# Kernel tuning notes

Measured on AMD Instinct MI355X. Metric: run time of the kernel, lower is better.

Reference implementation:

```python
import jax, jax.numpy as jnp
import numpy as np

EPS = 1e-5
NEG_SLOPE = 0.2  # DGL GATConv default leaky_relu slope


def conv1d_same(x, w, b):
    # x: [N, Cin, T], w: [Cout, Cin, K]
    y = jax.lax.conv_general_dilated(x, w, (1,), 'SAME',
                                     dimension_numbers=('NCW', 'OIW', 'NCW'))
    return y + b[None, :, None]


def gated_conv(x, w1, b1, w2, b2, w3, b3):
    # Temporal_Gated_Conv: relu(conv1(x)*sigmoid(conv2(x)) + conv3(x))
    return jax.nn.relu(conv1d_same(x, w1, b1) * jax.nn.sigmoid(conv1d_same(x, w2, b2))
                       + conv1d_same(x, w3, b3))


def bn3(x, g, b):
    # BatchNorm1d on [N, C, T]: stats over (N, T), training mode (batch stats)
    m = jnp.mean(x, (0, 2), keepdims=True)
    v = jnp.var(x, (0, 2), keepdims=True)
    return (x - m) * jax.lax.rsqrt(v + EPS) * g[None, :, None] + b[None, :, None]


def bn2(x, g, b):
    # BatchNorm1d on [N, F]: stats over N
    m = jnp.mean(x, 0, keepdims=True)
    v = jnp.var(x, 0, keepdims=True)
    return (x - m) * jax.lax.rsqrt(v + EPS) * g[None, :] + b[None, :]


def setup_inputs() -> dict:
    key = jax.random.key(0)
    ks = jax.random.split(key, 24)
    N, C, T, H, DEG = 20000, 32, 8, 4, 16
    F = C * T          # GAT in/out feats per head = 256
    E = N * DEG
    s = 0.05
    inp = {
        'X': jax.random.normal(ks[0], (N, C, T), jnp.float32),
        'src': jax.random.randint(ks[1], (E,), 0, N, jnp.int32),
        'dst': jax.random.randint(ks[2], (E,), 0, N, jnp.int32),
        # residual_proj: Conv1d(C->C, k=1)
        'rp_w': jax.random.normal(ks[3], (C, C, 1), jnp.float32) * s,
        'rp_b': jnp.zeros((C,), jnp.float32),
        # gated_conv1: three Conv1d(C->C, k=3)
        'g1_w1': jax.random.normal(ks[4], (C, C, 3), jnp.float32) * s,
        'g1_b1': jnp.zeros((C,), jnp.float32),
        'g1_w2': jax.random.normal(ks[5], (C, C, 3), jnp.float32) * s,
        'g1_b2': jnp.zeros((C,), jnp.float32),
        'g1_w3': jax.random.normal(ks[6], (C, C, 3), jnp.float32) * s,
        'g1_b3': jnp.zeros((C,), jnp.float32),
        'bn0_g': jnp.ones((C,), jnp.float32),
        'bn0_b': jnp.zeros((C,), jnp.float32),
        # GATConv: fc [H*F, F], attn_l/attn_r [H, F], bias [H*F]
        'gat_w': jax.random.normal(ks[7], (H * F, F), jnp.float32) * s,
        'attn_l': jax.random.normal(ks[8], (H, F), jnp.float32) * s,
        'attn_r': jax.random.normal(ks[9], (H, F), jnp.float32) * s,
        'gat_bias': jnp.zeros((H * F,), jnp.float32),
        'bn1_g': jnp.ones((H * F,), jnp.float32),
        'bn1_b': jnp.zeros((H * F,), jnp.float32),
        # gated_conv2: three Conv1d(C*H -> C, k=3)
        'g2_w1': jax.random.normal(ks[10], (C, C * H, 3), jnp.float32) * s,
        'g2_b1': jnp.zeros((C,), jnp.float32),
        'g2_w2': jax.random.normal(ks[11], (C, C * H, 3), jnp.float32) * s,
        'g2_b2': jnp.zeros((C,), jnp.float32),
        'g2_w3': jax.random.normal(ks[12], (C, C * H, 3), jnp.float32) * s,
        'g2_b3': jnp.zeros((C,), jnp.float32),
        'bn2_g': jnp.ones((C,), jnp.float32),
        'bn2_b': jnp.zeros((C,), jnp.float32),
    }
    return inp


def reference(X, src, dst, rp_w, rp_b, g1_w1, g1_b1, g1_w2, g1_b2, g1_w3, g1_b3,
              bn0_g, bn0_b, gat_w, attn_l, attn_r, gat_bias, bn1_g, bn1_b,
              g2_w1, g2_b1, g2_w2, g2_b2, g2_w3, g2_b3, bn2_g, bn2_b):
    N, C, T = X.shape
    H, F = attn_l.shape

    residual = conv1d_same(X, rp_w, rp_b)                      # [N, C, T]
    x = gated_conv(X, g1_w1, g1_b1, g1_w2, g1_b2, g1_w3, g1_b3)
    x = bn3(x, bn0_g, bn0_b)
    x = x.reshape(N, C * T)                                    # row-major flatten == torch .view

    # --- DGL GATConv (feat_drop=attn_drop=0, concat heads, ReLU activation) ---
    h = (x @ gat_w.T).reshape(N, H, F)                         # fc projection
    el = jnp.sum(h * attn_l, -1)                               # [N, H]
    er = jnp.sum(h * attn_r, -1)                               # [N, H]
    e = jax.nn.leaky_relu(el[src] + er[dst], NEG_SLOPE)        # [E, H]
    # segment softmax over incoming edges of each dst node
    m = jax.ops.segment_max(e, dst, num_segments=N)            # [N, H]
    ee = jnp.exp(e - m[dst])
    den = jax.ops.segment_sum(ee, dst, num_segments=N)         # [N, H]
    alpha = ee / den[dst]                                      # [E, H]
    rst = jax.ops.segment_sum(alpha[:, :, None] * h[src], dst, num_segments=N)  # [N, H, F]
    rst = jax.nn.relu(rst + gat_bias.reshape(H, F))

    x = rst.reshape(N, H * F)                                  # concat heads
    x = bn2(x, bn1_g, bn1_b)
    x = x.reshape(N, (H * F) // T, T)                          # [N, C*H, T]
    x = gated_conv(x, g2_w1, g2_b1, g2_w2, g2_b2, g2_w3, g2_b3)
    x = bn3(x, bn2_g, bn2_b)
    x = jax.nn.relu(x + residual)                              # self.last=True, dropout=0
    return x
```

## Files before the change

### kernel.cpp

```cpp
#include <hip/hip_runtime.h>
#include <stdint.h>

#define NN 20000
#define NE 320000

typedef unsigned short us16;
typedef __attribute__((ext_vector_type(8))) short short8;
typedef __attribute__((ext_vector_type(4))) float f32x4;

union U4 { uint4 v; us16 s[8]; unsigned u[4]; };
union U2 { uint2 v; us16 s[4]; };

__device__ __forceinline__ float b2f(us16 u){ return __uint_as_float(((unsigned)u)<<16); }
__device__ __forceinline__ us16 f2b(float f){
  unsigned u = __float_as_uint(f);
  u += 0x7fffu + ((u>>16)&1u);
  return (us16)(u>>16);
}

__global__ __launch_bounds__(256) void k_misc(
    const float* __restrict__ gatw, us16* __restrict__ Wb,
    const float* __restrict__ w1, const float* __restrict__ w2, const float* __restrict__ w3,
    us16* __restrict__ Wt,
    const float* __restrict__ c1w1, const float* __restrict__ c1w2, const float* __restrict__ c1w3,
    const float* __restrict__ rp_w, us16* __restrict__ Wt1,
    const float* __restrict__ attnl, const float* __restrict__ attnr,
    float* __restrict__ wl, float* __restrict__ wr,
    const int* __restrict__ dst, int* __restrict__ counts)
{
  const int b = blockIdx.x, tid = threadIdx.x;
  if(b < 256){
    int i = b*256 + tid;
    float4 v = *(const float4*)(gatw + (size_t)i*4);
    U2 o;
    o.s[0]=f2b(v.x); o.s[1]=f2b(v.y); o.s[2]=f2b(v.z); o.s[3]=f2b(v.w);
    *(uint2*)(Wb + (size_t)i*4) = o.v;
  } else if(b < 400){
    int i = (b-256)*256 + tid;
    int s = i/12288, rem = i%12288;
    int co3 = rem>>7, ci = rem&127;
    const float* w = (co3<32) ? w1 : (co3<64) ? w2 : w3;
    Wt[i] = f2b(w[(co3&31)*384 + ci*3 + s]);
  } else if(b < 448){
    int i = (b-400)*256 + tid;
    int s = i>>12, rem = i&4095;
    int co3 = rem>>5, ci = rem&31;
    float v;
    if(co3 < 96){
      const float* w = (co3<32) ? c1w1 : (co3<64) ? c1w2 : c1w3;
      v = w[(co3&31)*96 + ci*3 + s];
    } else {
      v = (s==1) ? rp_w[(co3-96)*32 + ci] : 0.f;
    }
    Wt1[i] = f2b(v);
  } else if(b < 480){
    int bb = b-448;
    int sel = bb>>4, hd = (bb>>2)&3, fq = bb&3;
    const float* attn = sel ? attnr : attnl;
    int k = tid;
    float s = 0.f;
    int f0 = fq*64;
    #pragma unroll 8
    for(int f=f0; f<f0+64; f++)
      s = fmaf(attn[hd*256+f], gatw[(size_t)(hd*256+f)*256 + k], s);
    atomicAdd(&((sel ? wr : wl)[hd*256+k]), s);
  } else {
    int e = (b-480)*256 + tid;
    if(e < NE) atomicAdd(&counts[dst[e]], 1);
  }
}

__global__ __launch_bounds__(256) void k_gemm1(
    const float* __restrict__ X, const us16* __restrict__ Wt1,
    const float* __restrict__ b1, const float* __restrict__ b2, const float* __restrict__ b3,
    const float* __restrict__ rp_b,
    us16* __restrict__ gc1, us16* __restrict__ resid,
    float* __restrict__ bn0_sum, float* __restrict__ bn0_sq,
    const int* __restrict__ counts, int* __restrict__ offsets, int* __restrict__ cursor)
{
  __shared__ float smemF[5760];
  __shared__ float redS[32], redQ[32];
  __shared__ int wred[4];
  const int tid = threadIdx.x;
  if(blockIdx.x < 1250){
    us16* As = (us16*)smemF;
    us16* Bs = As + 6400;
    if(tid<32){ redS[tid]=0.f; redQ[tid]=0.f; }
    const int node0 = blockIdx.x*16;
    const int lane = tid&63, wv = tid>>6;
    const int mrow = lane&15, kg = (lane>>4)*8;
    for(int idx=tid; idx<1024; idx+=256){
      int n = idx>>6, rem = idx&63, slot = (rem>>5)*9, ci = rem&31;
      As[n*400 + slot*40 + ci] = 0;
    }
    #pragma unroll
    for(int i=0;i<4;i++){
      int idx = i*256 + tid;
      int n = idx>>6, rem = idx&63, ci = rem>>1, tq = rem&1;
      float4 xv = *(const float4*)(X + (size_t)(node0+n)*256 + ci*8 + tq*4);
      us16* p = &As[n*400 + (tq*4+1)*40 + ci];
      p[0]   = f2b(xv.x);
      p[40]  = f2b(xv.y);
      p[80]  = f2b(xv.z);
      p[120] = f2b(xv.w);
    }
    f32x4 acc[2][8] = {};
    for(int s=0; s<3; s++){
      if(s) __syncthreads();
      #pragma unroll
      for(int i=0;i<2;i++){
        int c = i*256 + tid;
        int co = c>>2, cq = c&3;
        *(uint4*)&Bs[co*40 + cq*8] = *(const uint4*)(Wt1 + s*4096 + co*32 + cq*8);
      }
      __syncthreads();
      short8 af[2], bfr[8];
      #pragma unroll
      for(int i=0;i<2;i++){
        int r = wv*32 + i*16 + mrow;
        af[i] = *(const short8*)&As[(r>>3)*400 + ((r&7)+s)*40 + kg];
      }
      #pragma unroll
      for(int j=0;j<8;j++)
        bfr[j] = *(const short8*)&Bs[(j*16 + mrow)*40 + kg];
      #pragma unroll
      for(int i=0;i<2;i++){
        #pragma unroll
        for(int j=0;j<8;j++)
          acc[i][j] = __builtin_amdgcn_mfma_f32_16x16x32_bf16(af[i], bfr[j], acc[i][j], 0, 0, 0);
      }
    }
    __syncthreads();
    us16* Og = (us16*)smemF;
    us16* Or = Og + 4096;
    const int coA = lane&15, coB = coA+16;
    const float b1A=b1[coA], b2A=b2[coA], b3A=b3[coA], brA=rp_b[coA];
    const float b1B=b1[coB], b2B=b2[coB], b3B=b3[coB], brB=rp_b[coB];
    float sA=0.f, qA=0.f, sB=0.f, qB=0.f;
    const int g = lane>>4;
    #pragma unroll
    for(int i=0;i<2;i++){
      int node = wv*4 + i*2 + (g>>1);
      int t0 = (g&1)*4;
      U2 pA, pB, rA2, rB2;
      #pragma unroll
      for(int r=0;r<4;r++){
        float c1 = acc[i][0][r]+b1A, c2 = acc[i][2][r]+b2A, c3 = acc[i][4][r]+b3A;
        float rr = acc[i][6][r]+brA;
        float sg = 1.f/(1.f+__expf(-c2));
        float v = fmaf(c1,sg,c3); v = v>0.f ? v : 0.f;
        sA += v; qA += v*v;
        pA.s[r]=f2b(v); rA2.s[r]=f2b(rr);
        c1 = acc[i][1][r]+b1B; c2 = acc[i][3][r]+b2B; c3 = acc[i][5][r]+b3B;
        rr = acc[i][7][r]+brB;
        sg = 1.f/(1.f+__expf(-c2));
        v = fmaf(c1,sg,c3); v = v>0.f ? v : 0.f;
        sB += v; qB += v*v;
        pB.s[r]=f2b(v); rB2.s[r]=f2b(rr);
      }
      *(uint2*)&Og[node*256 + coA*8 + t0] = pA.v;
      *(uint2*)&Og[node*256 + coB*8 + t0] = pB.v;
      *(uint2*)&Or[node*256 + coA*8 + t0] = rA2.v;
      *(uint2*)&Or[node*256 + coB*8 + t0] = rB2.v;
    }
    sA += __shfl_xor(sA,16,64); sA += __shfl_xor(sA,32,64);
    qA += __shfl_xor(qA,16,64); qA += __shfl_xor(qA,32,64);
    sB += __shfl_xor(sB,16,64); sB += __shfl_xor(sB,32,64);
    qB += __shfl_xor(qB,16,64); qB += __shfl_xor(qB,32,64);
    if(lane < 16){
      atomicAdd(&redS[coA], sA); atomicAdd(&redQ[coA], qA);
      atomicAdd(&redS[coB], sB); atomicAdd(&redQ[coB], qB);
    }
    __syncthreads();
    #pragma unroll
    for(int i=0;i<2;i++){
      int idx = i*256 + tid;
      *(uint4*)(gc1   + (size_t)node0*256 + (size_t)idx*8) = *(const uint4*)&Og[idx*8];
      *(uint4*)(resid + (size_t)node0*256 + (size_t)idx*8) = *(const uint4*)&Or[idx*8];
    }
    if(tid<32)      atomicAdd(&bn0_sum[tid], redS[tid]);
    else if(tid<64) atomicAdd(&bn0_sq[tid-32], redQ[tid-32]);
  } else {
    const int lane = tid&63, wv = tid>>6;
    int running = 0;
    int4 cur;
    {
      int idx = tid*4;
      cur = *(const int4*)(counts + idx);
    }
    for(int t=0; t<20; t++){
      int4 nxt; nxt.x=0; nxt.y=0; nxt.z=0; nxt.w=0;
      if(t < 19){
        int idx = (t+1)*1024 + tid*4;
        if(idx+3 < NN) nxt = *(const int4*)(counts + idx);
        else {
          if(idx   < NN) nxt.x = counts[idx];
          if(idx+1 < NN) nxt.y = counts[idx+1];
          if(idx+2 < NN) nxt.z = counts[idx+2];
          if(idx+3 < NN) nxt.w = counts[idx+3];
        }
      }
      int s = cur.x + cur.y + cur.z + cur.w;
      int incl = s;
      #pragma unroll
      for(int off=1; off<64; off<<=1){
        int v = __shfl_up(incl, off, 64);
        if(lane >= off) incl += v;
      }
      if(lane==63) wred[wv] = incl;
      __syncthreads();
      int woff = 0, btot = 0;
      #pragma unroll
      for(int w2=0; w2<4; w2++){
        int x = wred[w2];
        btot += x;
        if(w2 < wv) woff += x;
      }
      int e0 = running + woff + incl - s;
      int idx = t*1024 + tid*4;
      int4 o; o.x=e0; o.y=e0+cur.x; o.z=o.y+cur.y; o.w=o.z+cur.z;
      if(idx+3 < NN){
        *(int4*)(offsets+idx) = o;
        *(int4*)(cursor+idx)  = o;
      } else {
        if(idx   < NN){ offsets[idx]  =o.x; cursor[idx]  =o.x; }
        if(idx+1 < NN){ offsets[idx+1]=o.y; cursor[idx+1]=o.y; }
        if(idx+2 < NN){ offsets[idx+2]=o.z; cursor[idx+2]=o.z; }
        if(idx+3 < NN){ offsets[idx+3]=o.w; cursor[idx+3]=o.w; }
      }
      running += btot;
      cur = nxt;
      __syncthreads();
    }
    if(tid==0) offsets[NN] = running;
  }
}

__global__ __launch_bounds__(256) void k_eler2(const us16* __restrict__ gc1,
    const float* __restrict__ bn0_sum, const float* __restrict__ bn0_sq,
    const float* __restrict__ bn0g, const float* __restrict__ bn0b,
    const float* __restrict__ wl, const float* __restrict__ wr,
    float* __restrict__ el, float* __restrict__ er)
{
  __shared__ float sa[32], sb[32];
  const int tid = threadIdx.x;
  if(tid<32){
    float m = bn0_sum[tid]*(1.f/160000.f);
    float v = bn0_sq[tid]*(1.f/160000.f) - m*m;
    float a = bn0g[tid]*rsqrtf(v + 1e-5f);
    sa[tid] = a; sb[tid] = bn0b[tid] - m*a;
  }
  __syncthreads();
  const int wv = tid>>6, lane = tid&63;
  const int node = blockIdx.x*4 + wv;
  U2 g; g.v = *(const uint2*)(gc1 + (size_t)node*256 + lane*4);
  const float a = sa[lane>>1], b = sb[lane>>1];
  float xv[4];
  #pragma unroll
  for(int j=0;j<4;j++) xv[j] = fmaf(a, b2f(g.s[j]), b);
  float res[8];
  #pragma unroll
  for(int hd=0; hd<4; hd++){
    float4 lv = *(const float4*)(wl + hd*256 + lane*4);
    float4 rv = *(const float4*)(wr + hd*256 + lane*4);
    res[hd]   = xv[0]*lv.x + xv[1]*lv.y + xv[2]*lv.z + xv[3]*lv.w;
    res[4+hd] = xv[0]*rv.x + xv[1]*rv.y + xv[2]*rv.z + xv[3]*rv.w;
  }
  #pragma unroll
  for(int o=32;o;o>>=1){
    #pragma unroll
    for(int k=0;k<8;k++) res[k] += __shfl_xor(res[k], o, 64);
  }
  if(lane==0){
    #pragma unroll
    for(int hd=0;hd<4;hd++){ el[node*4+hd]=res[hd]; er[node*4+hd]=res[4+hd]; }
  }
}

__global__ __launch_bounds__(256) void k_scatter(const int* __restrict__ src, const int* __restrict__ dst,
    int* __restrict__ cursor, int* __restrict__ esrc,
    const float* __restrict__ el, const float* __restrict__ er,
    float* __restrict__ ew)
{
  int e = blockIdx.x*256 + threadIdx.x;
  if(e < NE){
    int s = src[e], d = dst[e];
    int pos = atomicAdd(&cursor[d], 1);
    esrc[pos] = s;
    float4 lv = *(const float4*)(el + s*4);
    float4 rv = *(const float4*)(er + d*4);
    float4 sc;
    sc.x = lv.x+rv.x; sc.x = sc.x>0.f ? sc.x : 0.2f*sc.x;
    sc.y = lv.y+rv.y; sc.y = sc.y>0.f ? sc.y : 0.2f*sc.y;
    sc.z = lv.z+rv.z; sc.z = sc.z>0.f ? sc.z : 0.2f*sc.z;
    sc.w = lv.w+rv.w; sc.w = sc.w>0.f ? sc.w : 0.2f*sc.w;
    *(float4*)(ew + (size_t)pos*4) = sc;
  }
}

__global__ __launch_bounds__(256) void k_agg2(
    const int* __restrict__ offsets, const int* __restrict__ esrc,
    const float* __restrict__ ew, const us16* __restrict__ gc1,
    const float* __restrict__ bn0_sum, const float* __restrict__ bn0_sq,
    const float* __restrict__ bn0g, const float* __restrict__ bn0b,
    us16* __restrict__ Axg)
{
  const int tid = threadIdx.x;
  const int wv = tid>>6, lane = tid&63;
  const int node = blockIdx.x*4 + wv;
  const int ch = lane>>1;
  float mmn = bn0_sum[ch]*(1.f/160000.f);
  float vvn = bn0_sq[ch]*(1.f/160000.f) - mmn*mmn;
  float sa = bn0g[ch]*rsqrtf(vvn + 1e-5f);
  float sb = bn0b[ch] - mmn*sa;
  const int beg = offsets[node];
  const int deg = offsets[node+1] - beg;
  const int h = lane>>4, i0 = lane&15;
  float m = -3.0e38f;
  for(int i=i0; i<deg; i+=16) m = fmaxf(m, ew[(size_t)(beg+i)*4 + h]);
  m = fmaxf(m, __shfl_xor(m,1,64)); m = fmaxf(m, __shfl_xor(m,2,64));
  m = fmaxf(m, __shfl_xor(m,4,64)); m = fmaxf(m, __shfl_xor(m,8,64));
  float den = 0.f;
  for(int i=i0; i<deg; i+=16) den += __expf(ew[(size_t)(beg+i)*4 + h] - m);
  den += __shfl_xor(den,1,64); den += __shfl_xor(den,2,64);
  den += __shfl_xor(den,4,64); den += __shfl_xor(den,8,64);
  const float m0=__shfl(m,0,64),   m1=__shfl(m,16,64),  m2=__shfl(m,32,64),  m3=__shfl(m,48,64);
  const float d0=__shfl(den,0,64), d1=__shfl(den,16,64),d2=__shfl(den,32,64),d3=__shfl(den,48,64);
  const float v0=d0>0.f?1.f/d0:0.f, v1=d1>0.f?1.f/d1:0.f,
              v2=d2>0.f?1.f/d2:0.f, v3=d3>0.f?1.f/d3:0.f;
  float a0c[4]={},a1c[4]={},a2c[4]={},a3c[4]={};
  #pragma unroll 4
  for(int j=0; j<deg; j++){
    int pos = beg+j;
    float4 w4 = *(const float4*)(ew + (size_t)pos*4);
    int sN = esrc[pos];
    U2 hv; hv.v = *(const uint2*)(gc1 + (size_t)sN*256 + lane*4);
    float e0 = __expf(w4.x-m0)*v0;
    float e1 = __expf(w4.y-m1)*v1;
    float e2 = __expf(w4.z-m2)*v2;
    float e3 = __expf(w4.w-m3)*v3;
    #pragma unroll
    for(int kk=0;kk<4;kk++){
      float x = b2f(hv.s[kk]);
      a0c[kk] = fmaf(e0,x,a0c[kk]);
      a1c[kk] = fmaf(e1,x,a1c[kk]);
      a2c[kk] = fmaf(e2,x,a2c[kk]);
      a3c[kk] = fmaf(e3,x,a3c[kk]);
    }
  }
  const float sbi = sb * ((deg>0)?1.f:0.f);
  U2 o0,o1,o2,o3;
  #pragma unroll
  for(int kk=0;kk<4;kk++){
    o0.s[kk]=f2b(fmaf(sa,a0c[kk],sbi));
    o1.s[kk]=f2b(fmaf(sa,a1c[kk],sbi));
    o2.s[kk]=f2b(fmaf(sa,a2c[kk],sbi));
    o3.s[kk]=f2b(fmaf(sa,a3c[kk],sbi));
  }
  *(uint2*)(Axg + ((size_t)node)*256            + lane*4) = o0.v;
  *(uint2*)(Axg + ((size_t)NN + node)*256       + lane*4) = o1.v;
  *(uint2*)(Axg + ((size_t)2*NN + node)*256     + lane*4) = o2.v;
  *(uint2*)(Axg + ((size_t)3*NN + node)*256     + lane*4) = o3.v;
}

__global__ __launch_bounds__(256) void k_gemm3(const us16* __restrict__ Axg, const us16* __restrict__ Wb,
    const float* __restrict__ gbias, us16* __restrict__ rst,
    float* __restrict__ bn1_sum, float* __restrict__ bn1_sq)
{
  __shared__ us16 As[128*40];
  __shared__ us16 Bs[128*40];
  const int tid = threadIdx.x;
  const int row0 = blockIdx.x*128;
  const int cb   = blockIdx.y*128;
  const int hd   = blockIdx.z;
  const us16* A = Axg + (size_t)hd*NN*256;
  const us16* B = Wb  + (size_t)(hd*256 + cb)*256;
  const int lane = tid&63, wv = tid>>6;
  const int wm = wv&1, wn = wv>>1;
  const int mrow = lane&15, kg = (lane>>4)*8;
  f32x4 acc[4][4] = {};
  for(int k0=0; k0<256; k0+=32){
    #pragma unroll
    for(int i=0;i<2;i++){
      int chunk = i*256 + tid;
      int row = chunk>>2, cc = chunk&3;
      int g = row0 + row;
      uint4 av; av.x=0;av.y=0;av.z=0;av.w=0;
      if(g < NN) av = *(const uint4*)(A + (size_t)g*256 + k0 + cc*8);
      *(uint4*)&As[row*40 + cc*8] = av;
      *(uint4*)&Bs[row*40 + cc*8] = *(const uint4*)(B + (size_t)row*256 + k0 + cc*8);
    }
    __syncthreads();
    short8 af[4], bfr[4];
    #pragma unroll
    for(int i=0;i<4;i++) af[i]  = *(const short8*)&As[(wm*64 + i*16 + mrow)*40 + kg];
    #pragma unroll
    for(int j=0;j<4;j++) bfr[j] = *(const short8*)&Bs[(wn*64 + j*16 + mrow)*40 + kg];
    #pragma unroll
    for(int i=0;i<4;i++){
      #pragma unroll
      for(int j=0;j<4;j++)
        acc[i][j] = __builtin_amdgcn_mfma_f32_16x16x32_bf16(af[i], bfr[j], acc[i][j], 0, 0, 0);
    }
    __syncthreads();
  }
  float gb[4];
  #pragma unroll
  for(int j=0;j<4;j++)
    gb[j] = gbias[hd*256 + cb + wn*64 + j*16 + (lane&15)];
  float cs[4]={}, cq[4]={};
  #pragma unroll
  for(int i=0;i<4;i++){
    #pragma unroll
    for(int j=0;j<4;j++){
      #pragma unroll
      for(int r=0;r<4;r++){
        int g = row0 + wm*64 + i*16 + (lane>>4)*4 + r;
        if(g < NN){
          float v = acc[i][j][r] + gb[j];
          v = v>0.f ? v : 0.f;
          rst[(size_t)g*1024 + hd*256 + cb + wn*64 + j*16 + (lane&15)] = f2b(v);
          cs[j] += v; cq[j] += v*v;
        }
      }
    }
  }
  #pragma unroll
  for(int j=0;j<4;j++){
    cs[j] += __shfl_xor(cs[j],16,64); cs[j] += __shfl_xor(cs[j],32,64);
    cq[j] += __shfl_xor(cq[j],16,64); cq[j] += __shfl_xor(cq[j],32,64);
  }
  if(lane < 16){
    #pragma unroll
    for(int j=0;j<4;j++){
      int col = hd*256 + cb + wn*64 + j*16 + lane;
      atomicAdd(&bn1_sum[col], cs[j]);
      atomicAdd(&bn1_sq[col],  cq[j]);
    }
  }
}

__global__ __launch_bounds__(256) void k_gemm2(
    const us16* __restrict__ rst, const us16* __restrict__ Wt,
    const float* __restrict__ bn1_sum, const float* __restrict__ bn1_sq,
    const float* __restrict__ bn1g, const float* __restrict__ bn1b,
    const float* __restrict__ b1, const float* __restrict__ b2, const float* __restrict__ b3,
    us16* __restrict__ y2, float* __restrict__ bn2_sum, float* __restrict__ bn2_sq)
{
  __shared__ float smemF[12800];
  float* s1a = smemF;
  float* s1b = smemF + 1024;
  us16* As = (us16*)(smemF + 2048);
  us16* Bs = As + 11520;
  float* Cs = smemF;
  __shared__ float redS[32], redQ[32];
  const int tid = threadIdx.x;
  if(tid<32){ redS[tid]=0.f; redQ[tid]=0.f; }
  const int node0 = blockIdx.x*16;
  const int lane = tid&63, wv = tid>>6;
  const int wm = wv&1, wn = wv>>1;
  const int mrow = lane&15, kg = (lane>>4)*8;
  for(int f=tid; f<1024; f+=256){
    float m = bn1_sum[f]*(1.f/20000.f);
    float v = bn1_sq[f]*(1.f/20000.f) - m*m;
    float a = bn1g[f]*rsqrtf(v + 1e-5f);
    int l = (f&7)*128 + (f>>3);
    s1a[l] = a; s1b[l] = bn1b[f] - m*a;
  }
  for(int idx=tid; idx<2048; idx+=256){
    int n = idx>>7, rem = idx&127, slot = (rem>>6)*9, ci = rem&63;
    As[n*720 + slot*72 + ci] = 0;
  }
  __syncthreads();
  f32x4 acc[4][3] = {};
  for(int kc=0; kc<2; kc++){
    if(kc) __syncthreads();
    #pragma unroll
    for(int i=0;i<4;i++){
      int idx = i*256 + tid;
      int n = idx>>6, cil = idx&63;
      int ci = kc*64 + cil;
      U4 in; in.v = *(const uint4*)(rst + (size_t)(node0+n)*1024 + ci*8);
      us16* p = &As[n*720 + 72 + cil];
      #pragma unroll
      for(int t=0;t<8;t++){
        float a = s1a[t*128+ci], b = s1b[t*128+ci];
        p[t*72] = f2b(fmaf(a, b2f(in.s[t]), b));
      }
    }
    for(int s=0; s<3; s++){
      if(s) __syncthreads();
      #pragma unroll
      for(int i=0;i<3;i++){
        int chunk = i*256 + tid;
        int brow = chunk>>3, cc = chunk&7;
        *(uint4*)&Bs[brow*72 + cc*8] =
          *(const uint4*)(Wt + s*12288 + brow*128 + kc*64 + cc*8);
      }
      __syncthreads();
      #pragma unroll
      for(int kk=0; kk<64; kk+=32){
        short8 af[4], bfr[3];
        #pragma unroll
        for(int i=0;i<4;i++){
          int r = wm*64 + i*16 + mrow;
          af[i] = *(const short8*)&As[(r>>3)*720 + ((r&7)+s)*72 + kk + kg];
        }
        #pragma unroll
        for(int j=0;j<3;j++)
          bfr[j] = *(const short8*)&Bs[(wn*48 + j*16 + mrow)*72 + kk + kg];
        #pragma unroll
        for(int i=0;i<4;i++){
          #pragma unroll
          for(int j=0;j<3;j++)
            acc[i][j] = __builtin_amdgcn_mfma_f32_16x16x32_bf16(af[i], bfr[j], acc[i][j], 0, 0, 0);
        }
      }
    }
  }
  __syncthreads();
  #pragma unroll
  for(int i=0;i<4;i++){
    #pragma unroll
    for(int j=0;j<3;j++){
      #pragma unroll
      for(int r=0;r<4;r++)
        Cs[(wm*64 + i*16 + (lane>>4)*4 + r)*100 + wn*48 + j*16 + (lane&15)] = acc[i][j][r];
    }
  }
  __syncthreads();
  const int co = tid&31, rg = tid>>5;
  const float bb1=b1[co], bb2=b2[co], bb3=b3[co];
  float s=0.f, q=0.f;
  #pragma unroll
  for(int half=0; half<2; half++){
    U4 ov;
    #pragma unroll
    for(int t=0;t<8;t++){
      int r = rg*16 + half*8 + t;
      float c1 = Cs[r*100 + co]      + bb1;
      float c2 = Cs[r*100 + co + 32] + bb2;
      float c3 = Cs[r*100 + co + 64] + bb3;
      float sg = 1.f/(1.f+__expf(-c2));
      float v = fmaf(c1, sg, c3);
      v = v>0.f ? v : 0.f;
      s += v; q += v*v;
      ov.s[t] = f2b(v);
    }
    int node = node0 + rg*2 + half;
    *(uint4*)(y2 + (size_t)node*256 + co*8) = ov.v;
  }
  atomicAdd(&redS[co], s); atomicAdd(&redQ[co], q);
  __syncthreads();
  if(tid<32)      atomicAdd(&bn2_sum[tid], redS[tid]);
  else if(tid<64) atomicAdd(&bn2_sq[tid-32], redQ[tid-32]);
}

__global__ __launch_bounds__(256) void k_final(const us16* __restrict__ y2,
    const float* __restrict__ bn2_sum, const float* __restrict__ bn2_sq,
    const float* __restrict__ bn2g, const float* __restrict__ bn2b,
    const us16* __restrict__ resid, float* __restrict__ out)
{
  __shared__ float fa[32], fb[32];
  const int tid = threadIdx.x;
  if(tid<32){
    float m = bn2_sum[tid]*(1.f/160000.f);
    float v = bn2_sq[tid]*(1.f/160000.f) - m*m;
    float a = bn2g[tid]*rsqrtf(v + 1e-5f);
    fa[tid] = a; fb[tid] = bn2b[tid] - m*a;
  }
  __syncthreads();
  size_t base = ((size_t)blockIdx.x*256 + tid)*8;
  int ch = (int)((base>>3)&31);
  float a = fa[ch], b = fb[ch];
  U4 yv, rv;
  yv.v = *(const uint4*)(y2+base);
  rv.v = *(const uint4*)(resid+base);
  float4 o0, o1;
  float vv[8];
  #pragma unroll
  for(int j=0;j<8;j++){
    float v = fmaf(a, b2f(yv.s[j]), b) + b2f(rv.s[j]);
    vv[j] = v>0.f ? v : 0.f;
  }
  o0.x=vv[0]; o0.y=vv[1]; o0.z=vv[2]; o0.w=vv[3];
  o1.x=vv[4]; o1.y=vv[5]; o1.z=vv[6]; o1.w=vv[7];
  *(float4*)(out+base)   = o0;
  *(float4*)(out+base+4) = o1;
}

extern "C" void kernel_launch(void* const* d_in, const int* in_sizes, int n_in,
                              void* d_out, int out_size, void* d_ws, size_t ws_size,
                              hipStream_t stream)
{
  const float* X    = (const float*)d_in[0];
  const int*  src   = (const int*)d_in[1];
  const int*  dst   = (const int*)d_in[2];
  const float* rp_w = (const float*)d_in[3];
  const float* rp_b = (const float*)d_in[4];
  const float* g1w1 = (const float*)d_in[5];
  const float* g1b1 = (const float*)d_in[6];
  const float* g1w2 = (const float*)d_in[7];
  const float* g1b2 = (const float*)d_in[8];
  const float* g1w3 = (const float*)d_in[9];
  const float* g1b3 = (const float*)d_in[10];
  const float* bn0g = (const float*)d_in[11];
  const float* bn0b = (const float*)d_in[12];
  const float* gatw = (const float*)d_in[13];
  const float* attnl= (const float*)d_in[14];
  const float* attnr= (const float*)d_in[15];
  const float* gbias= (const float*)d_in[16];
  const float* bn1g = (const float*)d_in[17];
  const float* bn1b = (const float*)d_in[18];
  const float* g2w1 = (const float*)d_in[19];
  const float* g2b1 = (const float*)d_in[20];
  const float* g2w2 = (const float*)d_in[21];
  const float* g2b2 = (const float*)d_in[22];
  const float* g2w3 = (const float*)d_in[23];
  const float* g2b3 = (const float*)d_in[24];
  const float* bn2g = (const float*)d_in[25];
  const float* bn2b = (const float*)d_in[26];
  float* out = (float*)d_out;
  (void)in_sizes; (void)n_in; (void)out_size; (void)ws_size;

  char* w = (char*)d_ws;
  float* bn0_sum = (float*)w;
  float* bn0_sq  = bn0_sum + 32;
  float* bn1_sum = bn0_sum + 64;
  float* bn1_sq  = bn1_sum + 1024;
  float* bn2_sum = bn1_sq  + 1024;
  float* bn2_sq  = bn2_sum + 32;
  float* wl      = bn2_sq + 32;
  float* wr      = wl + 1024;
  int*   counts  = (int*)(wr + 1024);
  size_t zeroBytes = (size_t)((char*)(counts + NN) - w);
  int*   offsets = counts + NN;
  int*   cursor  = offsets + 20004;
  int*   esrc    = cursor + NN;
  float* el      = (float*)(esrc + NE);
  float* er      = el + NN*4;
  float* ew      = er + NN*4;
  us16*  wb      = (us16*)(ew + (size_t)NE*4);
  us16*  resid   = wb + 262144;
  us16*  gc1     = resid + 5120000;
  us16*  Axg     = gc1   + 5120000;
  us16*  rst     = Axg   + 20480000;
  us16*  Wt      = rst   + 20480000;
  us16*  Wt1     = Wt    + 36864;
  us16*  y2      = gc1;

  hipMemsetAsync(d_ws, 0, zeroBytes, stream);
  k_misc<<<1730, 256, 0, stream>>>(gatw, wb, g2w1, g2w2, g2w3, Wt,
                                   g1w1, g1w2, g1w3, rp_w, Wt1,
                                   attnl, attnr, wl, wr, dst, counts);
  k_gemm1<<<1251, 256, 0, stream>>>(X, Wt1, g1b1, g1b2, g1b3, rp_b,
                                    gc1, resid, bn0_sum, bn0_sq,
                                    counts, offsets, cursor);
  k_eler2<<<5000, 256, 0, stream>>>(gc1, bn0_sum, bn0_sq, bn0g, bn0b, wl, wr, el, er);
  k_scatter<<<1250, 256, 0, stream>>>(src, dst, cursor, esrc, el, er, ew);
  k_agg2<<<5000, 256, 0, stream>>>(offsets, esrc, ew, gc1, bn0_sum, bn0_sq, bn0g, bn0b, Axg);
  k_gemm3<<<dim3(157, 2, 4), 256, 0, stream>>>(Axg, wb, gbias, rst, bn1_sum, bn1_sq);
  k_gemm2<<<1250, 256, 0, stream>>>(rst, Wt, bn1_sum, bn1_sq, bn1g, bn1b,
                                    g2b1, g2b2, g2b3, y2, bn2_sum, bn2_sq);
  k_final<<<2500, 256, 0, stream>>>(y2, bn2_sum, bn2_sq, bn2g, bn2b, resid, out);
}
```

Before: 363.4 us.

## Register-prefetch next K tiles in GAT GEMM and gated-conv GEMM kernels

The GAT projection GEMM now stages 64-wide K tiles through a wider LDS buffer and prefetches the next tile from global memory into registers while the MFMAs run on the current one. The main loop also drops from 8 to 4 iterations, which removes half of the barriers. The gated-conv GEMM gets the same treatment: it preloads the rst input chunks and the weight tiles into registers one stage ahead. The aim is to hide global load latency behind compute, at the cost of more registers and more LDS, which may lower occupancy.

Result: slower. 401.1 us (+10.4%).

```diff
diff --git a/kernel.cpp b/kernel.cpp
--- a/kernel.cpp
+++ b/kernel.cpp
@@ -367,8 +367,8 @@
     const float* __restrict__ gbias, us16* __restrict__ rst,
     float* __restrict__ bn1_sum, float* __restrict__ bn1_sq)
 {
-  __shared__ us16 As[128*40];
-  __shared__ us16 Bs[128*40];
+  __shared__ us16 As[128*72];
+  __shared__ us16 Bs[128*72];
   const int tid = threadIdx.x;
   const int row0 = blockIdx.x*128;
   const int cb   = blockIdx.y*128;
@@ -378,31 +378,53 @@
   const int lane = tid&63, wv = tid>>6;
   const int wm = wv&1, wn = wv>>1;
   const int mrow = lane&15, kg = (lane>>4)*8;
+  const int srow = tid>>3, scc = tid&7;
+  uint4 apre[4], bpre[4];
+  #pragma unroll
+  for(int i=0;i<4;i++){
+    int row = i*32 + srow;
+    int g = row0 + row;
+    uint4 av; av.x=0;av.y=0;av.z=0;av.w=0;
+    if(g < NN) av = *(const uint4*)(A + (size_t)g*256 + scc*8);
+    apre[i] = av;
+    bpre[i] = *(const uint4*)(B + (size_t)row*256 + scc*8);
+  }
   f32x4 acc[4][4] = {};
-  for(int k0=0; k0<256; k0+=32){
-    #pragma unroll
-    for(int i=0;i<2;i++){
-      int chunk = i*256 + tid;
-      int row = chunk>>2, cc = chunk&3;
-      int g = row0 + row;
-      uint4 av; av.x=0;av.y=0;av.z=0;av.w=0;
-      if(g < NN) av = *(const uint4*)(A + (size_t)g*256 + k0 + cc*8);
-      *(uint4*)&As[row*40 + cc*8] = av;
-      *(uint4*)&Bs[row*40 + cc*8] = *(const uint4*)(B + (size_t)row*256 + k0 + cc*8);
+  for(int it=0; it<4; it++){
+    if(it) __syncthreads();
+    #pragma unroll
+    for(int i=0;i<4;i++){
+      int row = i*32 + srow;
+      *(uint4*)&As[row*72 + scc*8] = apre[i];
+      *(uint4*)&Bs[row*72 + scc*8] = bpre[i];
     }
     __syncthreads();
-    short8 af[4], bfr[4];
-    #pragma unroll
-    for(int i=0;i<4;i++) af[i]  = *(const short8*)&As[(wm*64 + i*16 + mrow)*40 + kg];
-    #pragma unroll
-    for(int j=0;j<4;j++) bfr[j] = *(const short8*)&Bs[(wn*64 + j*16 + mrow)*40 + kg];
-    #pragma unroll
-    for(int i=0;i<4;i++){
-      #pragma unroll
-      for(int j=0;j<4;j++)
-        acc[i][j] = __builtin_amdgcn_mfma_f32_16x16x32_bf16(af[i], bfr[j], acc[i][j], 0, 0, 0);
-    }
-    __syncthreads();
+    if(it < 3){
+      int k0 = (it+1)*64;
+      #pragma unroll
+      for(int i=0;i<4;i++){
+        int row = i*32 + srow;
+        int g = row0 + row;
+        uint4 av; av.x=0;av.y=0;av.z=0;av.w=0;
+        if(g < NN) av = *(const uint4*)(A + (size_t)g*256 + k0 + scc*8);
+        apre[i] = av;
+        bpre[i] = *(const uint4*)(B + (size_t)row*256 + k0 + scc*8);
+      }
+    }
+    #pragma unroll
+    for(int kk=0; kk<64; kk+=32){
+      short8 af[4], bfr[4];
+      #pragma unroll
+      for(int i=0;i<4;i++) af[i]  = *(const short8*)&As[(wm*64 + i*16 + mrow)*72 + kk + kg];
+      #pragma unroll
+      for(int j=0;j<4;j++) bfr[j] = *(const short8*)&Bs[(wn*64 + j*16 + mrow)*72 + kk + kg];
+      #pragma unroll
+      for(int i=0;i<4;i++){
+        #pragma unroll
+        for(int j=0;j<4;j++)
+          acc[i][j] = __builtin_amdgcn_mfma_f32_16x16x32_bf16(af[i], bfr[j], acc[i][j], 0, 0, 0);
+      }
+    }
   }
   float gb[4];
   #pragma unroll
@@ -460,6 +482,19 @@
   const int lane = tid&63, wv = tid>>6;
   const int wm = wv&1, wn = wv>>1;
   const int mrow = lane&15, kg = (lane>>4)*8;
+  uint4 apre[4], bpre[3];
+  #pragma unroll
+  for(int i=0;i<4;i++){
+    int idx = i*256 + tid;
+    int n = idx>>6, cil = idx&63;
+    apre[i] = *(const uint4*)(rst + (size_t)(node0+n)*1024 + cil*8);
+  }
+  #pragma unroll
+  for(int i=0;i<3;i++){
+    int chunk = i*256 + tid;
+    int brow = chunk>>3, cc = chunk&7;
+    bpre[i] = *(const uint4*)(Wt + brow*128 + cc*8);
+  }
   for(int f=tid; f<1024; f+=256){
     float m = bn1_sum[f]*(1.f/20000.f);
     float v = bn1_sq[f]*(1.f/20000.f) - m*m;
@@ -480,7 +515,7 @@
       int idx = i*256 + tid;
       int n = idx>>6, cil = idx&63;
       int ci = kc*64 + cil;
-      U4 in; in.v = *(const uint4*)(rst + (size_t)(node0+n)*1024 + ci*8);
+      U4 in; in.v = apre[i];
       us16* p = &As[n*720 + 72 + cil];
       #pragma unroll
       for(int t=0;t<8;t++){
@@ -488,16 +523,33 @@
         p[t*72] = f2b(fmaf(a, b2f(in.s[t]), b));
       }
     }
+    if(kc==0){
+      #pragma unroll
+      for(int i=0;i<4;i++){
+        int idx = i*256 + tid;
+        int n = idx>>6, cil = idx&63;
+        apre[i] = *(const uint4*)(rst + (size_t)(node0+n)*1024 + 512 + cil*8);
+      }
+    }
     for(int s=0; s<3; s++){
       if(s) __syncthreads();
       #pragma unroll
       for(int i=0;i<3;i++){
         int chunk = i*256 + tid;
         int brow = chunk>>3, cc = chunk&7;
-        *(uint4*)&Bs[brow*72 + cc*8] =
-          *(const uint4*)(Wt + s*12288 + brow*128 + kc*64 + cc*8);
+        *(uint4*)&Bs[brow*72 + cc*8] = bpre[i];
       }
       __syncthreads();
+      int nst = kc*3 + s + 1;
+      if(nst < 6){
+        int kcn = nst/3, sn = nst%3;
+        #pragma unroll
+        for(int i=0;i<3;i++){
+          int chunk = i*256 + tid;
+          int brow = chunk>>3, cc = chunk&7;
+          bpre[i] = *(const uint4*)(Wt + sn*12288 + brow*128 + kcn*64 + cc*8);
+        }
+      }
       #pragma unroll
       for(int kk=0; kk<64; kk+=32){
         short8 af[4], bfr[3];
```

## Load GEMM operands directly from global memory and restructure gated-conv epilogue in registers

Applied to the files above, without the earlier changes.

The GAT fc GEMM kernel stops staging A/B tiles in shared memory and loads MFMA fragments straight from global memory, which drops both per-iteration barriers. The gated conv kernel reads weight fragments directly from global, remaps waves so each one owns all 96 output columns for 32 rows, and fuses bias, sigmoid gating and BN statistics in registers using shuffles. Its output is staged as bf16 in shared memory for coalesced stores, which shrinks LDS use. The cost is uncoalesced, narrower global loads that depend on L1/L2 hits, and more per-lane loads.

New measurement: 396.8 us. 9.2% more time.

```diff
diff --git a/kernel.cpp b/kernel.cpp
--- a/kernel.cpp
+++ b/kernel.cpp
@@ -367,8 +367,6 @@
     const float* __restrict__ gbias, us16* __restrict__ rst,
     float* __restrict__ bn1_sum, float* __restrict__ bn1_sq)
 {
-  __shared__ us16 As[128*40];
-  __shared__ us16 Bs[128*40];
   const int tid = threadIdx.x;
   const int row0 = blockIdx.x*128;
   const int cb   = blockIdx.y*128;
@@ -378,31 +376,26 @@
   const int lane = tid&63, wv = tid>>6;
   const int wm = wv&1, wn = wv>>1;
   const int mrow = lane&15, kg = (lane>>4)*8;
+  const short8 zz = {0,0,0,0,0,0,0,0};
+  int ga[4];
+  #pragma unroll
+  for(int i=0;i<4;i++) ga[i] = row0 + wm*64 + i*16 + mrow;
   f32x4 acc[4][4] = {};
+  #pragma unroll 2
   for(int k0=0; k0<256; k0+=32){
-    #pragma unroll
-    for(int i=0;i<2;i++){
-      int chunk = i*256 + tid;
-      int row = chunk>>2, cc = chunk&3;
-      int g = row0 + row;
-      uint4 av; av.x=0;av.y=0;av.z=0;av.w=0;
-      if(g < NN) av = *(const uint4*)(A + (size_t)g*256 + k0 + cc*8);
-      *(uint4*)&As[row*40 + cc*8] = av;
-      *(uint4*)&Bs[row*40 + cc*8] = *(const uint4*)(B + (size_t)row*256 + k0 + cc*8);
-    }
-    __syncthreads();
     short8 af[4], bfr[4];
     #pragma unroll
-    for(int i=0;i<4;i++) af[i]  = *(const short8*)&As[(wm*64 + i*16 + mrow)*40 + kg];
-    #pragma unroll
-    for(int j=0;j<4;j++) bfr[j] = *(const short8*)&Bs[(wn*64 + j*16 + mrow)*40 + kg];
+    for(int i=0;i<4;i++)
+      af[i] = (ga[i] < NN) ? *(const short8*)(A + (size_t)ga[i]*256 + k0 + kg) : zz;
+    #pragma unroll
+    for(int j=0;j<4;j++)
+      bfr[j] = *(const short8*)(B + (size_t)(wn*64 + j*16 + mrow)*256 + k0 + kg);
     #pragma unroll
     for(int i=0;i<4;i++){
       #pragma unroll
       for(int j=0;j<4;j++)
         acc[i][j] = __builtin_amdgcn_mfma_f32_16x16x32_bf16(af[i], bfr[j], acc[i][j], 0, 0, 0);
     }
-    __syncthreads();
   }
   float gb[4];
   #pragma unroll
@@ -447,18 +440,15 @@
     const float* __restrict__ b1, const float* __restrict__ b2, const float* __restrict__ b3,
     us16* __restrict__ y2, float* __restrict__ bn2_sum, float* __restrict__ bn2_sq)
 {
-  __shared__ float smemF[12800];
+  __shared__ float smemF[7808];
   float* s1a = smemF;
   float* s1b = smemF + 1024;
   us16* As = (us16*)(smemF + 2048);
-  us16* Bs = As + 11520;
-  float* Cs = smemF;
   __shared__ float redS[32], redQ[32];
   const int tid = threadIdx.x;
   if(tid<32){ redS[tid]=0.f; redQ[tid]=0.f; }
   const int node0 = blockIdx.x*16;
   const int lane = tid&63, wv = tid>>6;
-  const int wm = wv&1, wn = wv>>1;
   const int mrow = lane&15, kg = (lane>>4)*8;
   for(int f=tid; f<1024; f+=256){
     float m = bn1_sum[f]*(1.f/20000.f);
@@ -472,7 +462,7 @@
     As[n*720 + slot*72 + ci] = 0;
   }
   __syncthreads();
-  f32x4 acc[4][3] = {};
+  f32x4 acc[2][6] = {};
   for(int kc=0; kc<2; kc++){
     if(kc) __syncthreads();
     #pragma unroll
@@ -488,70 +478,69 @@
         p[t*72] = f2b(fmaf(a, b2f(in.s[t]), b));
       }
     }
+    __syncthreads();
+    #pragma unroll
     for(int s=0; s<3; s++){
-      if(s) __syncthreads();
-      #pragma unroll
-      for(int i=0;i<3;i++){
-        int chunk = i*256 + tid;
-        int brow = chunk>>3, cc = chunk&7;
-        *(uint4*)&Bs[brow*72 + cc*8] =
-          *(const uint4*)(Wt + s*12288 + brow*128 + kc*64 + cc*8);
-      }
-      __syncthreads();
       #pragma unroll
       for(int kk=0; kk<64; kk+=32){
-        short8 af[4], bfr[3];
+        short8 af[2], bfr[6];
         #pragma unroll
-        for(int i=0;i<4;i++){
-          int r = wm*64 + i*16 + mrow;
+        for(int i=0;i<2;i++){
+          int r = wv*32 + i*16 + mrow;
           af[i] = *(const short8*)&As[(r>>3)*720 + ((r&7)+s)*72 + kk + kg];
         }
         #pragma unroll
-        for(int j=0;j<3;j++)
-          bfr[j] = *(const short8*)&Bs[(wn*48 + j*16 + mrow)*72 + kk + kg];
+        for(int j=0;j<6;j++)
+          bfr[j] = *(const short8*)(Wt + s*12288 + (j*16 + mrow)*128 + kc*64 + kk + kg);
         #pragma unroll
-        for(int i=0;i<4;i++){
+        for(int i=0;i<2;i++){
           #pragma unroll
-          for(int j=0;j<3;j++)
+          for(int j=0;j<6;j++)
             acc[i][j] = __builtin_amdgcn_mfma_f32_16x16x32_bf16(af[i], bfr[j], acc[i][j], 0, 0, 0);
         }
       }
     }
   }
   __syncthreads();
-  #pragma unroll
-  for(int i=0;i<4;i++){
-    #pragma unroll
-    for(int j=0;j<3;j++){
-      #pragma unroll
-      for(int r=0;r<4;r++)
-        Cs[(wm*64 + i*16 + (lane>>4)*4 + r)*100 + wn*48 + j*16 + (lane&15)] = acc[i][j][r];
-    }
+  us16* Og = (us16*)smemF;
+  const int coA = lane&15, coB = coA+16;
+  const float b1A=b1[coA], b2A=b2[coA], b3A=b3[coA];
+  const float b1B=b1[coB], b2B=b2[coB], b3B=b3[coB];
+  float sA=0.f, qA=0.f, sB=0.f, qB=0.f;
+  const int g = lane>>4;
+  #pragma unroll
+  for(int i=0;i<2;i++){
+    int node = wv*4 + i*2 + (g>>1);
+    int t0 = (g&1)*4;
+    U2 pA, pB;
+    #pragma unroll
+    for(int r=0;r<4;r++){
+      float c1 = acc[i][0][r]+b1A, c2 = acc[i][2][r]+b2A, c3 = acc[i][4][r]+b3A;
+      float sg = 1.f/(1.f+__expf(-c2));
+      float v = fmaf(c1,sg,c3); v = v>0.f ? v : 0.f;
+      sA += v; qA += v*v; pA.s[r]=f2b(v);
+      c1 = acc[i][1][r]+b1B; c2 = acc[i][3][r]+b2B; c3 = acc[i][5][r]+b3B;
+      sg = 1.f/(1.f+__expf(-c2));
+      v = fmaf(c1,sg,c3); v = v>0.f ? v : 0.f;
+      sB += v; qB += v*v; pB.s[r]=f2b(v);
+    }
+    *(uint2*)&Og[node*256 + coA*8 + t0] = pA.v;
+    *(uint2*)&Og[node*256 + coB*8 + t0] = pB.v;
+  }
+  sA += __shfl_xor(sA,16,64); sA += __shfl_xor(sA,32,64);
+  qA += __shfl_xor(qA,16,64); qA += __shfl_xor(qA,32,64);
+  sB += __shfl_xor(sB,16,64); sB += __shfl_xor(sB,32,64);
+  qB += __shfl_xor(qB,16,64); qB += __shfl_xor(qB,32,64);
+  if(lane < 16){
+    atomicAdd(&redS[coA], sA); atomicAdd(&redQ[coA], qA);
+    atomicAdd(&redS[coB], sB); atomicAdd(&redQ[coB], qB);
   }
   __syncthreads();
-  const int co = tid&31, rg = tid>>5;
-  const float bb1=b1[co], bb2=b2[co], bb3=b3[co];
-  float s=0.f, q=0.f;
-  #pragma unroll
-  for(int half=0; half<2; half++){
-    U4 ov;
-    #pragma unroll
-    for(int t=0;t<8;t++){
-      int r = rg*16 + half*8 + t;
-      float c1 = Cs[r*100 + co]      + bb1;
-      float c2 = Cs[r*100 + co + 32] + bb2;
-      float c3 = Cs[r*100 + co + 64] + bb3;
-      float sg = 1.f/(1.f+__expf(-c2));
-      float v = fmaf(c1, sg, c3);
-      v = v>0.f ? v : 0.f;
-      s += v; q += v*v;
-      ov.s[t] = f2b(v);
-    }
-    int node = node0 + rg*2 + half;
-    *(uint4*)(y2 + (size_t)node*256 + co*8) = ov.v;
-  }
-  atomicAdd(&redS[co], s); atomicAdd(&redQ[co], q);
-  __syncthreads();
+  #pragma unroll
+  for(int i=0;i<2;i++){
+    int idx = i*256 + tid;
+    *(uint4*)(y2 + (size_t)node0*256 + (size_t)idx*8) = *(const uint4*)&Og[idx*8];
+  }
   if(tid<32)      atomicAdd(&bn2_sum[tid], redS[tid]);
   else if(tid<64) atomicAdd(&bn2_sq[tid-32], redQ[tid-32]);
 }
```
